# Performance work log

Hardware: AMD Instinct MI355X
Metric: run time of the kernel (lower is better)

Reference implementation:

```python
import jax, jax.numpy as jnp
import numpy as np

B, N = 16, 64
EMB, CDIM, NL = 32, 24, 3      # emb_dim, cloud_dim, number of degrees l=0..2 (cloudord)
NBASIS, H, RADIUS = 10, 150, 2.0
BETA = 5.0                     # rescaled_act.Softplus(beta=5)


def sp(x):
    return jax.nn.softplus(BETA * x) / BETA


def cosine_basis(r):
    # CosineBasisModel: cos^2 bumps on centers linspace(0, max_radius, nbasis)
    centers = jnp.linspace(0.0, RADIUS, NBASIS).astype(r.dtype)
    step = RADIUS / (NBASIS - 1)
    d = (r[..., None] - centers) / step
    return jnp.where(jnp.abs(d) < 1.0, jnp.cos(0.5 * jnp.pi * d) ** 2, 0.0)


def sph_harm(u):
    # real spherical harmonics l=0,1,2 on unit vectors u[...,3]
    x, y, z = u[..., 0], u[..., 1], u[..., 2]
    Y0 = jnp.full(u.shape[:-1] + (1,), 0.28209479177387814, u.dtype)
    c1 = 0.4886025119029199
    Y1 = c1 * jnp.stack([y, z, x], -1)
    c2a, c2b, c2c = 1.0925484305920792, 0.31539156525252005, 0.5462742152960396
    Y2 = jnp.stack([c2a * x * y, c2a * y * z, c2b * (3 * z * z - 1.0),
                    c2a * x * z, c2c * (x * x - y * y)], -1)
    return [Y0, Y1, Y2]


def setup_inputs() -> dict:
    key = jax.random.key(0)
    ks = jax.random.split(key, 16)
    d = {}
    d['xyz'] = jax.random.normal(ks[0], (B, N, 3), jnp.float32)
    d['Z'] = jax.random.randint(ks[1], (B, N), 0, 6)
    d['body23'] = jax.random.normal(ks[2], (B, N, 3), jnp.float32)
    # embedding table (6 species)
    d['emb_W'] = jax.random.normal(ks[3], (6, EMB), jnp.float32) * 0.1
    # radial model MLP: NBASIS -> 150 -> 150 -> 150 -> NL*CDIM*EMB
    ROUT = NL * CDIM * EMB
    d['rW0'] = jax.random.normal(ks[4], (NBASIS, H), jnp.float32) / np.sqrt(NBASIS)
    d['rb0'] = jnp.zeros((H,), jnp.float32)
    d['rW1'] = jax.random.normal(ks[5], (H, H), jnp.float32) / np.sqrt(H)
    d['rb1'] = jnp.zeros((H,), jnp.float32)
    d['rW2'] = jax.random.normal(ks[6], (H, H), jnp.float32) / np.sqrt(H)
    d['rb2'] = jnp.zeros((H,), jnp.float32)
    d['rW3'] = jax.random.normal(ks[7], (H, ROUT), jnp.float32) / np.sqrt(H)
    d['rb3'] = jnp.zeros((ROUT,), jnp.float32)
    # AtomResiduals (1 block) on 219 channels
    CR = CDIM * NL * NL + 3  # 219
    d['res_W'] = jax.random.normal(ks[8], (CR, CR), jnp.float32) / np.sqrt(CR)
    d['res_b'] = jnp.zeros((CR,), jnp.float32)
    # collate: Linear(438,128) + BatchNorm1d(128)
    d['c_W'] = jax.random.normal(ks[9], (2 * CR, 128), jnp.float32) / np.sqrt(2 * CR)
    d['c_b'] = jnp.zeros((128,), jnp.float32)
    d['bn_g'] = jnp.ones((128,), jnp.float32)
    d['bn_b'] = jnp.zeros((128,), jnp.float32)
    # output layer
    d['o_W'] = jax.random.normal(ks[10], (128, 1), jnp.float32) / np.sqrt(128.0)
    d['o_b'] = jnp.zeros((1,), jnp.float32)
    return d


def reference(xyz, Z, body23, emb_W, rW0, rb0, rW1, rb1, rW2, rb2, rW3, rb3,
              res_W, res_b, c_W, c_b, bn_g, bn_b, o_W, o_b):
    f = emb_W[Z]                                        # [B,N,EMB] atom embeddings
    diff = xyz[:, :, None, :] - xyz[:, None, :, :]      # [B,N,N,3]
    r = jnp.sqrt(jnp.sum(diff * diff, -1) + 1e-12)      # [B,N,N]
    mask = ((r < RADIUS) & (r > 1e-6)).astype(f.dtype)  # neighbors within radius, no self
    u = diff / r[..., None]
    Ys = sph_harm(u)                                    # [ [B,N,N,1], [..,3], [..,5] ]
    # radial model on all pairs
    h = sp(cosine_basis(r) @ rW0 + rb0)
    h = sp(h @ rW1 + rb1)
    h = sp(h @ rW2 + rb2)
    R = (h @ rW3 + rb3).reshape(B, N, N, NL, CDIM, EMB)
    R = R * mask[..., None, None, None]
    # equivariant neighbor convolution: out[a,co,l,m] = sum_n,ci R_l(r_an) Y_lm(u_an) f[n,ci]
    outs = []
    for l in range(NL):
        o = jnp.einsum('banoi,banm,bni->baom', R[..., l, :, :], Ys[l], f)
        outs.append(o.reshape(B, N, -1) / jnp.sqrt(float(N)))
    feats = jnp.concatenate(outs, -1)                   # [B,N,216]
    feats = jnp.concatenate([body23, feats], -1)        # [B,N,219] (final_res concat)
    # AtomResiduals: concat(x, x + sp(Linear(x))) -> channel doubling
    res = feats + sp(feats @ res_W + res_b)
    feats = jnp.concatenate([feats, res], -1)           # [B,N,438]
    # lp_pool2d(norm_type=2, kernel=(N,1)): sqrt of sum of squares over atoms
    pooled = jnp.sqrt(jnp.sum(feats * feats, axis=1))   # [B,438]
    # collate: softplus(Linear), softplus(BatchNorm1d) (training-mode batch stats)
    hh = jax.nn.softplus(pooled @ c_W + c_b)
    mu = hh.mean(0)
    var = hh.var(0)
    hh = jax.nn.softplus((hh - mu) / jnp.sqrt(var + 1e-5) * bn_g + bn_b)
    return jax.nn.sigmoid(hh @ o_W + o_b)               # [B,1]
```

## Files before the change

### kernel.cpp

```cpp
#include <hip/hip_runtime.h>
#include <math.h>

constexpr int cB  = 16;
constexpr int cN  = 64;
constexpr int EMB = 32;
constexpr int NL  = 3;
constexpr int CDIM = 24;
constexpr int LOD = NL * CDIM;
constexpr int NB  = 10;
constexpr int H   = 150;
constexpr int CR  = 219;
constexpr int C2  = 438;
constexpr int HD  = 128;
constexpr int NSP = 6;
constexpr int GC  = NSP * LOD;
constexpr int GCP = 512;
constexpr int TBL = 512;
constexpr float RADIUS = 2.0f;

__device__ __forceinline__ float sp5(float x) {
    return fmaxf(x, 0.0f) + 0.2f * log1pf(expf(-5.0f * fabsf(x)));
}
__device__ __forceinline__ float sp1(float x) {
    return fmaxf(x, 0.0f) + log1pf(expf(-fabsf(x)));
}

__global__ void __launch_bounds__(256) k_prep(const float* __restrict__ emb_W,
                                              const float* __restrict__ rW3,
                                              const float* __restrict__ rb3,
                                              const float* __restrict__ rW0,
                                              const float* __restrict__ rW1,
                                              const float* __restrict__ rW2,
                                              const float* __restrict__ c_W,
                                              float* __restrict__ W2,
                                              float* __restrict__ Pbz,
                                              float* __restrict__ rW0p,
                                              float* __restrict__ rW1p,
                                              float* __restrict__ rW2p,
                                              float* __restrict__ c_Wt) {
    int bx = blockIdx.x;
    int t = threadIdx.x;
    __shared__ float e[EMB];
    if (bx < 90) {
        int z = bx / 15, hb = bx - (bx / 15) * 15;
        if (t < EMB) e[t] = emb_W[z * EMB + t];
        __syncthreads();
        for (int o = t; o < 10 * LOD; o += 256) {
            int k = hb * 10 + o / LOD, lo = o % LOD;
            const float* wr = &rW3[(size_t)k * (LOD * EMB) + lo * EMB];
            float s = 0.0f;
            #pragma unroll
            for (int i = 0; i < EMB; ++i) s = fmaf(wr[i], e[i], s);
            W2[(size_t)k * GCP + z * LOD + lo] = s;
        }
        if (z == 0) {
            for (int o = t; o < 10 * (GCP - GC); o += 256) {
                int k = hb * 10 + o / (GCP - GC), c = GC + o % (GCP - GC);
                W2[(size_t)k * GCP + c] = 0.0f;
            }
        }
        if (hb == 0 && t < LOD) {
            float s = 0.0f;
            #pragma unroll
            for (int i = 0; i < EMB; ++i) s = fmaf(rb3[t * EMB + i], e[i], s);
            Pbz[z * LOD + t] = s;
        }
    } else {
        int pb = bx - 90;
        int total = NB * 152 + 2 * H * 152 + HD * 440;
        for (int i = pb * 256 + t; i < total; i += 256 * 256) {
            if (i < NB * 152) {
                int r = i / 152, c = i - r * 152;
                rW0p[i] = (c < H) ? rW0[r * H + c] : 0.0f;
            } else if (i < NB * 152 + H * 152) {
                int j = i - NB * 152; int r = j / 152, c = j - r * 152;
                rW1p[j] = (c < H) ? rW1[r * H + c] : 0.0f;
            } else if (i < NB * 152 + 2 * H * 152) {
                int j = i - NB * 152 - H * 152; int r = j / 152, c = j - r * 152;
                rW2p[j] = (c < H) ? rW2[r * H + c] : 0.0f;
            } else {
                int j = i - NB * 152 - 2 * H * 152;
                int jj = j / 440, ch = j - jj * 440;
                c_Wt[j] = (ch < C2) ? c_W[ch * HD + jj] : 0.0f;
            }
        }
    }
}

__global__ void __launch_bounds__(256) k_chain(const float* __restrict__ rW0p,
                                               const float* __restrict__ rb0,
                                               const float* __restrict__ rW1p,
                                               const float* __restrict__ rb1,
                                               const float* __restrict__ rW2p,
                                               const float* __restrict__ rb2,
                                               const float* __restrict__ W2,
                                               const float* __restrict__ Pbz,
                                               float* __restrict__ G) {
    const int row0 = blockIdx.x * 2;
    const int t = threadIdx.x;
    const int a2 = t >> 7;
    const int jt = t & 127;
    const bool hasx = (jt < 22);
    const int jx = hasx ? 128 + jt : 128;

    __shared__ __align__(16) float bas[2][10];
    __shared__ __align__(16) float hA[2 * 152];
    __shared__ __align__(16) float hB[2 * 152];

    if (t < 2) {
        float r = (float)(row0 + t) * (RADIUS / (float)(TBL - 1));
        #pragma unroll
        for (int k = 0; k < NB; ++k) {
            float d = r * 4.5f - (float)k;
            float v = 0.0f;
            if (fabsf(d) < 1.0f) { float cc = cosf(1.57079632679489662f * d); v = cc * cc; }
            bas[t][k] = v;
        }
    }
    __syncthreads();

    {
        float a0 = 0, ax = 0;
        #pragma unroll
        for (int k = 0; k < NB; ++k) {
            float x = bas[a2][k];
            a0 = fmaf(x, rW0p[k * 152 + jt], a0);
            ax = fmaf(x, rW0p[k * 152 + jx], ax);
        }
        hA[a2 * 152 + jt] = sp5(a0 + rb0[jt]);
        if (hasx) hA[a2 * 152 + 128 + jt] = sp5(ax + rb0[128 + jt]);
    }
    __syncthreads();

    for (int layer = 0; layer < 2; ++layer) {
        const float* W   = layer ? rW2p : rW1p;
        const float* bb  = layer ? rb2 : rb1;
        const float* src = layer ? hB : hA;
        float*       dst = layer ? hA : hB;
        float a0 = 0, ax = 0;
        const float* xs = &src[a2 * 152];
        #pragma unroll 10
        for (int k = 0; k < H; ++k) {
            float x = xs[k];
            const float* wr = &W[k * 152];
            a0 = fmaf(x, wr[jt], a0);
            ax = fmaf(x, wr[jx], ax);
        }
        dst[a2 * 152 + jt] = sp5(a0 + bb[jt]);
        if (hasx) dst[a2 * 152 + 128 + jt] = sp5(ax + bb[128 + jt]);
        __syncthreads();
    }

    if (jt < 108) {
        const int g0 = 4 * jt;
        float4 c0 = {0, 0, 0, 0};
        const float* xs = &hA[a2 * 152];
        #pragma unroll 10
        for (int k = 0; k < H; ++k) {
            float x = xs[k];
            float4 w = *(const float4*)&W2[(size_t)k * GCP + g0];
            c0.x = fmaf(x, w.x, c0.x); c0.y = fmaf(x, w.y, c0.y);
            c0.z = fmaf(x, w.z, c0.z); c0.w = fmaf(x, w.w, c0.w);
        }
        int row = row0 + a2;
        float4 p = *(const float4*)&Pbz[g0];
        float4 o;
        o.x = c0.x + p.x; o.y = c0.y + p.y; o.z = c0.z + p.z; o.w = c0.w + p.w;
        *(float4*)&G[(size_t)row * GC + g0] = o;
    }
}

__global__ void __launch_bounds__(256) k_red(const float* __restrict__ xyz,
                                             const int* __restrict__ Z,
                                             const float* __restrict__ body23,
                                             const float* __restrict__ G,
                                             const float* __restrict__ res_W,
                                             const float* __restrict__ res_b,
                                             float* __restrict__ feats) {
    int ba = blockIdx.x;
    int b = ba >> 6, a = ba & 63;
    int t = threadIdx.x;
    __shared__ float ym[64][12];
    __shared__ float ps[64][76];
    __shared__ float xr[CR];
    __shared__ int t0s[64];
    __shared__ float wls[64];
    __shared__ int zs[64];
    __shared__ int msks[64];
    if (t < 64) {
        int n = t;
        float ax = xyz[((size_t)b * cN + a) * 3 + 0];
        float ay = xyz[((size_t)b * cN + a) * 3 + 1];
        float az = xyz[((size_t)b * cN + a) * 3 + 2];
        float d0 = ax - xyz[((size_t)b * cN + n) * 3 + 0];
        float d1 = ay - xyz[((size_t)b * cN + n) * 3 + 1];
        float d2 = az - xyz[((size_t)b * cN + n) * 3 + 2];
        float s = d0 * d0 + d1 * d1 + d2 * d2;
        float r = sqrtf(s + 1e-12f);
        msks[n] = (r < RADIUS) && (r > 1e-6f);
        float u = r * ((float)(TBL - 1) / RADIUS);
        int t0 = (int)u;
        if (t0 > TBL - 2) t0 = TBL - 2;
        t0s[n] = t0;
        wls[n] = u - (float)t0;
        zs[n] = Z[b * cN + n];
        float inv = 1.0f / r;
        float x = d0 * inv, y = d1 * inv, z = d2 * inv;
        ym[n][0] = 0.28209479177387814f;
        ym[n][1] = 0.4886025119029199f * y;
        ym[n][2] = 0.4886025119029199f * z;
        ym[n][3] = 0.4886025119029199f * x;
        ym[n][4] = 1.0925484305920792f * x * y;
        ym[n][5] = 1.0925484305920792f * y * z;
        ym[n][6] = 0.31539156525252005f * (3.0f * z * z - 1.0f);
        ym[n][7] = 1.0925484305920792f * x * z;
        ym[n][8] = 0.5462742152960396f * (x * x - y * y);
    }
    __syncthreads();
    for (int i = t; i < 64 * LOD; i += 256) {
        int n = i / LOD, lo = i - n * LOD;
        float v = 0.0f;
        if (msks[n]) {
            const float* g = &G[(size_t)t0s[n] * GC + zs[n] * LOD + lo];
            float g0 = g[0], g1 = g[GC];
            v = g0 + wls[n] * (g1 - g0);
        }
        ps[n][lo] = v;
    }
    __syncthreads();
    if (t < 216) {
        int lo, yi;
        if (t < 24) { lo = t; yi = 0; }
        else if (t < 96) { int q = t - 24; int o = q / 3; lo = 24 + o; yi = 1 + (q - o * 3); }
        else { int q = t - 96; int o = q / 5; lo = 48 + o; yi = 4 + (q - o * 5); }
        float acc = 0.0f;
        #pragma unroll 4
        for (int n = 0; n < cN; ++n)
            acc = fmaf(ps[n][lo], ym[n][yi], acc);
        xr[3 + t] = acc * 0.125f;
    } else if (t < 219) {
        xr[t - 216] = body23[(size_t)ba * 3 + (t - 216)];
    }
    __syncthreads();
    if (t < CR) {
        float xv = xr[t];
        feats[(size_t)ba * C2 + t] = xv;
        float r0 = 0.0f, r1 = 0.0f, r2 = 0.0f;
        #pragma unroll 3
        for (int k = 0; k < CR; k += 3) {
            r0 = fmaf(xr[k + 0], res_W[(k + 0) * CR + t], r0);
            r1 = fmaf(xr[k + 1], res_W[(k + 1) * CR + t], r1);
            r2 = fmaf(xr[k + 2], res_W[(k + 2) * CR + t], r2);
        }
        float racc = res_b[t] + ((r0 + r1) + r2);
        feats[(size_t)ba * C2 + CR + t] = xv + sp5(racc);
    }
}

__global__ void __launch_bounds__(64) k_pool(const float* __restrict__ feats,
                                             float* __restrict__ pooled) {
    int b = blockIdx.x;
    int ch = blockIdx.y * 64 + threadIdx.x;
    if (ch < C2) {
        float s = 0.0f;
        #pragma unroll 4
        for (int a = 0; a < cN; ++a) {
            float v = feats[(size_t)(b * cN + a) * C2 + ch];
            s = fmaf(v, v, s);
        }
        pooled[b * C2 + ch] = sqrtf(s);
    }
}

__global__ void __launch_bounds__(64) k_head1(const float* __restrict__ pooled,
                                              const float* __restrict__ c_Wt,
                                              const float* __restrict__ c_b,
                                              float* __restrict__ hh) {
    int j = blockIdx.x;
    int l = threadIdx.x;
    float acc[cB];
    #pragma unroll
    for (int b = 0; b < cB; ++b) acc[b] = 0.0f;
    const float* wr = &c_Wt[j * 440];
    for (int ch = l; ch < C2; ch += 64) {
        float wv = wr[ch];
        #pragma unroll
        for (int b = 0; b < cB; ++b)
            acc[b] = fmaf(pooled[b * C2 + ch], wv, acc[b]);
    }
    #pragma unroll
    for (int off = 32; off >= 1; off >>= 1) {
        #pragma unroll
        for (int b = 0; b < cB; ++b) acc[b] += __shfl_xor(acc[b], off, 64);
    }
    if (l == 0) {
        float cb = c_b[j];
        #pragma unroll
        for (int b = 0; b < cB; ++b) hh[b * HD + j] = sp1(acc[b] + cb);
    }
}

__global__ void __launch_bounds__(128) k_head2(const float* __restrict__ hh,
                                               const float* __restrict__ bn_g,
                                               const float* __restrict__ bn_b,
                                               const float* __restrict__ o_W,
                                               const float* __restrict__ o_b,
                                               float* __restrict__ out) {
    __shared__ float hh2[cB][HD];
    int t = threadIdx.x;
    float v[cB];
    float mu = 0.0f;
    #pragma unroll
    for (int b = 0; b < cB; ++b) { v[b] = hh[b * HD + t]; mu += v[b]; }
    mu *= (1.0f / cB);
    float var = 0.0f;
    #pragma unroll
    for (int b = 0; b < cB; ++b) { float d = v[b] - mu; var = fmaf(d, d, var); }
    var *= (1.0f / cB);
    float sc = bn_g[t] / sqrtf(var + 1e-5f);
    float bnb = bn_b[t];
    #pragma unroll
    for (int b = 0; b < cB; ++b) hh2[b][t] = sp1((v[b] - mu) * sc + bnb);
    __syncthreads();
    if (t < cB) {
        float s = o_b[0];
        for (int j = 0; j < HD; ++j) s = fmaf(hh2[t][j], o_W[j], s);
        out[t] = 1.0f / (1.0f + expf(-s));
    }
}

extern "C" void kernel_launch(void* const* d_in, const int* in_sizes, int n_in,
                              void* d_out, int out_size, void* d_ws, size_t ws_size,
                              hipStream_t stream) {
    const float* xyz    = (const float*)d_in[0];
    const int*   Z      = (const int*)d_in[1];
    const float* body23 = (const float*)d_in[2];
    const float* emb_W  = (const float*)d_in[3];
    const float* rW0    = (const float*)d_in[4];
    const float* rb0    = (const float*)d_in[5];
    const float* rW1    = (const float*)d_in[6];
    const float* rb1    = (const float*)d_in[7];
    const float* rW2    = (const float*)d_in[8];
    const float* rb2    = (const float*)d_in[9];
    const float* rW3    = (const float*)d_in[10];
    const float* rb3    = (const float*)d_in[11];
    const float* res_W  = (const float*)d_in[12];
    const float* res_b  = (const float*)d_in[13];
    const float* c_W    = (const float*)d_in[14];
    const float* c_b    = (const float*)d_in[15];
    const float* bn_g   = (const float*)d_in[16];
    const float* bn_b   = (const float*)d_in[17];
    const float* o_W    = (const float*)d_in[18];
    const float* o_b    = (const float*)d_in[19];

    float* w      = (float*)d_ws;
    float* W2     = w;
    float* Pbz    = W2 + 76800;
    float* rW0p   = Pbz + 432;
    float* rW1p   = rW0p + 1520;
    float* rW2p   = rW1p + 22800;
    float* c_Wt   = rW2p + 22800;
    float* G      = c_Wt + 56320;
    float* feats  = G + 221184;
    float* pooled = feats + 448512;
    float* hh     = pooled + 7008;
    (void)in_sizes; (void)n_in; (void)out_size; (void)ws_size;

    k_prep <<<346, 256, 0, stream>>>(emb_W, rW3, rb3, rW0, rW1, rW2, c_W,
                                     W2, Pbz, rW0p, rW1p, rW2p, c_Wt);
    k_chain<<<TBL / 2, 256, 0, stream>>>(rW0p, rb0, rW1p, rb1, rW2p, rb2, W2, Pbz, G);
    k_red  <<<cB * cN, 256, 0, stream>>>(xyz, Z, body23, G, res_W, res_b, feats);
    k_pool <<<dim3(cB, 7), 64, 0, stream>>>(feats, pooled);
    k_head1<<<HD, 64, 0, stream>>>(pooled, c_Wt, c_b, hh);
    k_head2<<<1, 128, 0, stream>>>(hh, bn_g, bn_b, o_W, o_b, (float*)d_out);
}
```

Before: 73.82 us.

## Fuse atom pooling into reduction kernel via atomics and process two atoms per block

New measurement: 75.54 us. +2.3%, slower.

```diff
diff --git a/kernel.cpp b/kernel.cpp
--- a/kernel.cpp
+++ b/kernel.cpp
@@ -37,7 +37,8 @@
                                               float* __restrict__ rW0p,
                                               float* __restrict__ rW1p,
                                               float* __restrict__ rW2p,
-                                              float* __restrict__ c_Wt) {
+                                              float* __restrict__ c_Wt,
+                                              float* __restrict__ pooled2) {
     int bx = blockIdx.x;
     int t = threadIdx.x;
     __shared__ float e[EMB];
@@ -68,7 +69,8 @@
     } else {
         int pb = bx - 90;
         int total = NB * 152 + 2 * H * 152 + HD * 440;
-        for (int i = pb * 256 + t; i < total; i += 256 * 256) {
+        int total2 = total + cB * C2;
+        for (int i = pb * 256 + t; i < total2; i += 256 * 256) {
             if (i < NB * 152) {
                 int r = i / 152, c = i - r * 152;
                 rW0p[i] = (c < H) ? rW0[r * H + c] : 0.0f;
@@ -78,10 +80,12 @@
             } else if (i < NB * 152 + 2 * H * 152) {
                 int j = i - NB * 152 - H * 152; int r = j / 152, c = j - r * 152;
                 rW2p[j] = (c < H) ? rW2[r * H + c] : 0.0f;
-            } else {
+            } else if (i < total) {
                 int j = i - NB * 152 - 2 * H * 152;
                 int jj = j / 440, ch = j - jj * 440;
                 c_Wt[j] = (ch < C2) ? c_W[ch * HD + jj] : 0.0f;
+            } else {
+                pooled2[i - total] = 0.0f;
             }
         }
     }
@@ -176,103 +180,96 @@
                                              const float* __restrict__ G,
                                              const float* __restrict__ res_W,
                                              const float* __restrict__ res_b,
-                                             float* __restrict__ feats) {
-    int ba = blockIdx.x;
-    int b = ba >> 6, a = ba & 63;
+                                             float* __restrict__ pooled2) {
+    int bp = blockIdx.x;
+    int b = bp >> 5;
+    int apair = (bp & 31) * 2;
     int t = threadIdx.x;
     __shared__ float ym[64][12];
     __shared__ float ps[64][76];
-    __shared__ float xr[CR];
+    __shared__ float xr2[2][224];
     __shared__ int t0s[64];
     __shared__ float wls[64];
     __shared__ int zs[64];
     __shared__ int msks[64];
-    if (t < 64) {
-        int n = t;
-        float ax = xyz[((size_t)b * cN + a) * 3 + 0];
-        float ay = xyz[((size_t)b * cN + a) * 3 + 1];
-        float az = xyz[((size_t)b * cN + a) * 3 + 2];
-        float d0 = ax - xyz[((size_t)b * cN + n) * 3 + 0];
-        float d1 = ay - xyz[((size_t)b * cN + n) * 3 + 1];
-        float d2 = az - xyz[((size_t)b * cN + n) * 3 + 2];
-        float s = d0 * d0 + d1 * d1 + d2 * d2;
-        float r = sqrtf(s + 1e-12f);
-        msks[n] = (r < RADIUS) && (r > 1e-6f);
-        float u = r * ((float)(TBL - 1) / RADIUS);
-        int t0 = (int)u;
-        if (t0 > TBL - 2) t0 = TBL - 2;
-        t0s[n] = t0;
-        wls[n] = u - (float)t0;
-        zs[n] = Z[b * cN + n];
-        float inv = 1.0f / r;
-        float x = d0 * inv, y = d1 * inv, z = d2 * inv;
-        ym[n][0] = 0.28209479177387814f;
-        ym[n][1] = 0.4886025119029199f * y;
-        ym[n][2] = 0.4886025119029199f * z;
-        ym[n][3] = 0.4886025119029199f * x;
-        ym[n][4] = 1.0925484305920792f * x * y;
-        ym[n][5] = 1.0925484305920792f * y * z;
-        ym[n][6] = 0.31539156525252005f * (3.0f * z * z - 1.0f);
-        ym[n][7] = 1.0925484305920792f * x * z;
-        ym[n][8] = 0.5462742152960396f * (x * x - y * y);
-    }
-    __syncthreads();
-    for (int i = t; i < 64 * LOD; i += 256) {
-        int n = i / LOD, lo = i - n * LOD;
-        float v = 0.0f;
-        if (msks[n]) {
-            const float* g = &G[(size_t)t0s[n] * GC + zs[n] * LOD + lo];
-            float g0 = g[0], g1 = g[GC];
-            v = g0 + wls[n] * (g1 - g0);
-        }
-        ps[n][lo] = v;
-    }
-    __syncthreads();
-    if (t < 216) {
-        int lo, yi;
-        if (t < 24) { lo = t; yi = 0; }
-        else if (t < 96) { int q = t - 24; int o = q / 3; lo = 24 + o; yi = 1 + (q - o * 3); }
-        else { int q = t - 96; int o = q / 5; lo = 48 + o; yi = 4 + (q - o * 5); }
-        float acc = 0.0f;
-        #pragma unroll 4
-        for (int n = 0; n < cN; ++n)
-            acc = fmaf(ps[n][lo], ym[n][yi], acc);
-        xr[3 + t] = acc * 0.125f;
-    } else if (t < 219) {
-        xr[t - 216] = body23[(size_t)ba * 3 + (t - 216)];
-    }
-    __syncthreads();
+
+    for (int aa = 0; aa < 2; ++aa) {
+        int a = apair + aa;
+        if (t < 64) {
+            int n = t;
+            float ax = xyz[((size_t)b * cN + a) * 3 + 0];
+            float ay = xyz[((size_t)b * cN + a) * 3 + 1];
+            float az = xyz[((size_t)b * cN + a) * 3 + 2];
+            float d0 = ax - xyz[((size_t)b * cN + n) * 3 + 0];
+            float d1 = ay - xyz[((size_t)b * cN + n) * 3 + 1];
+            float d2 = az - xyz[((size_t)b * cN + n) * 3 + 2];
+            float s = d0 * d0 + d1 * d1 + d2 * d2;
+            float r = sqrtf(s + 1e-12f);
+            msks[n] = (r < RADIUS) && (r > 1e-6f);
+            float u = r * ((float)(TBL - 1) / RADIUS);
+            int t0 = (int)u;
+            if (t0 > TBL - 2) t0 = TBL - 2;
+            t0s[n] = t0;
+            wls[n] = u - (float)t0;
+            zs[n] = Z[b * cN + n];
+            float inv = 1.0f / r;
+            float x = d0 * inv, y = d1 * inv, z = d2 * inv;
+            ym[n][0] = 0.28209479177387814f;
+            ym[n][1] = 0.4886025119029199f * y;
+            ym[n][2] = 0.4886025119029199f * z;
+            ym[n][3] = 0.4886025119029199f * x;
+            ym[n][4] = 1.0925484305920792f * x * y;
+            ym[n][5] = 1.0925484305920792f * y * z;
+            ym[n][6] = 0.31539156525252005f * (3.0f * z * z - 1.0f);
+            ym[n][7] = 1.0925484305920792f * x * z;
+            ym[n][8] = 0.5462742152960396f * (x * x - y * y);
+        }
+        __syncthreads();
+        for (int i = t; i < 64 * LOD; i += 256) {
+            int n = i / LOD, lo = i - n * LOD;
+            float v = 0.0f;
+            if (msks[n]) {
+                const float* g = &G[(size_t)t0s[n] * GC + zs[n] * LOD + lo];
+                float g0 = g[0], g1 = g[GC];
+                v = g0 + wls[n] * (g1 - g0);
+            }
+            ps[n][lo] = v;
+        }
+        __syncthreads();
+        if (t < 216) {
+            int lo, yi;
+            if (t < 24) { lo = t; yi = 0; }
+            else if (t < 96) { int q = t - 24; int o = q / 3; lo = 24 + o; yi = 1 + (q - o * 3); }
+            else { int q = t - 96; int o = q / 5; lo = 48 + o; yi = 4 + (q - o * 5); }
+            float acc = 0.0f;
+            #pragma unroll 4
+            for (int n = 0; n < cN; ++n)
+                acc = fmaf(ps[n][lo], ym[n][yi], acc);
+            xr2[aa][3 + t] = acc * 0.125f;
+        } else if (t < 219) {
+            xr2[aa][t - 216] = body23[(size_t)(b * cN + a) * 3 + (t - 216)];
+        }
+        __syncthreads();
+    }
+
     if (t < CR) {
-        float xv = xr[t];
-        feats[(size_t)ba * C2 + t] = xv;
-        float r0 = 0.0f, r1 = 0.0f, r2 = 0.0f;
+        float xv0 = xr2[0][t], xv1 = xr2[1][t];
+        float s0 = 0.0f, s1 = 0.0f;
         #pragma unroll 3
-        for (int k = 0; k < CR; k += 3) {
-            r0 = fmaf(xr[k + 0], res_W[(k + 0) * CR + t], r0);
-            r1 = fmaf(xr[k + 1], res_W[(k + 1) * CR + t], r1);
-            r2 = fmaf(xr[k + 2], res_W[(k + 2) * CR + t], r2);
-        }
-        float racc = res_b[t] + ((r0 + r1) + r2);
-        feats[(size_t)ba * C2 + CR + t] = xv + sp5(racc);
-    }
-}
-
-__global__ void __launch_bounds__(64) k_pool(const float* __restrict__ feats,
-                                             float* __restrict__ pooled) {
-    int b = blockIdx.x;
-    int ch = blockIdx.y * 64 + threadIdx.x;
-    if (ch < C2) {
-        float s = 0.0f;
-        #pragma unroll 4
-        for (int a = 0; a < cN; ++a) {
-            float v = feats[(size_t)(b * cN + a) * C2 + ch];
-            s = fmaf(v, v, s);
-        }
-        pooled[b * C2 + ch] = sqrtf(s);
-    }
-}
-
-__global__ void __launch_bounds__(64) k_head1(const float* __restrict__ pooled,
+        for (int k = 0; k < CR; ++k) {
+            float w = res_W[(size_t)k * CR + t];
+            s0 = fmaf(xr2[0][k], w, s0);
+            s1 = fmaf(xr2[1][k], w, s1);
+        }
+        float rb = res_b[t];
+        float o0 = xv0 + sp5(rb + s0);
+        float o1 = xv1 + sp5(rb + s1);
+        atomicAdd(&pooled2[b * C2 + t],       xv0 * xv0 + xv1 * xv1);
+        atomicAdd(&pooled2[b * C2 + CR + t],  o0 * o0 + o1 * o1);
+    }
+}
+
+__global__ void __launch_bounds__(64) k_head1(const float* __restrict__ pooled2,
                                               const float* __restrict__ c_Wt,
                                               const float* __restrict__ c_b,
                                               float* __restrict__ hh) {
@@ -286,7 +283,7 @@
         float wv = wr[ch];
         #pragma unroll
         for (int b = 0; b < cB; ++b)
-            acc[b] = fmaf(pooled[b * C2 + ch], wv, acc[b]);
+            acc[b] = fmaf(sqrtf(pooled2[b * C2 + ch]), wv, acc[b]);
     }
     #pragma unroll
     for (int off = 32; off >= 1; off >>= 1) {
@@ -353,24 +350,22 @@
     const float* o_W    = (const float*)d_in[18];
     const float* o_b    = (const float*)d_in[19];
 
-    float* w      = (float*)d_ws;
-    float* W2     = w;
-    float* Pbz    = W2 + 76800;
-    float* rW0p   = Pbz + 432;
-    float* rW1p   = rW0p + 1520;
-    float* rW2p   = rW1p + 22800;
-    float* c_Wt   = rW2p + 22800;
-    float* G      = c_Wt + 56320;
-    float* feats  = G + 221184;
-    float* pooled = feats + 448512;
-    float* hh     = pooled + 7008;
+    float* w       = (float*)d_ws;
+    float* W2      = w;
+    float* Pbz     = W2 + 76800;
+    float* rW0p    = Pbz + 432;
+    float* rW1p    = rW0p + 1520;
+    float* rW2p    = rW1p + 22800;
+    float* c_Wt    = rW2p + 22800;
+    float* G       = c_Wt + 56320;
+    float* pooled2 = G + 221184;
+    float* hh      = pooled2 + 7008;
     (void)in_sizes; (void)n_in; (void)out_size; (void)ws_size;
 
     k_prep <<<346, 256, 0, stream>>>(emb_W, rW3, rb3, rW0, rW1, rW2, c_W,
-                                     W2, Pbz, rW0p, rW1p, rW2p, c_Wt);
+                                     W2, Pbz, rW0p, rW1p, rW2p, c_Wt, pooled2);
     k_chain<<<TBL / 2, 256, 0, stream>>>(rW0p, rb0, rW1p, rb1, rW2p, rb2, W2, Pbz, G);
-    k_red  <<<cB * cN, 256, 0, stream>>>(xyz, Z, body23, G, res_W, res_b, feats);
-    k_pool <<<dim3(cB, 7), 64, 0, stream>>>(feats, pooled);
-    k_head1<<<HD, 64, 0, stream>>>(pooled, c_Wt, c_b, hh);
+    k_red  <<<cB * cN / 2, 256, 0, stream>>>(xyz, Z, body23, G, res_W, res_b, pooled2);
+    k_head1<<<HD, 64, 0, stream>>>(pooled2, c_Wt, c_b, hh);
     k_head2<<<1, 128, 0, stream>>>(hh, bn_g, bn_b, o_W, o_b, (float*)d_out);
 }
```
